# Kernel tuning notes

Hardware: AMD Instinct MI355X
Metric: run time of the kernel (lower is better)

The kernel has to match this reference:

```python
import jax, jax.numpy as jnp
import numpy as np

B, S, IN_DIM, D, H, L, C = 8, 1024, 256, 1024, 16, 6, 10
DK = D // H
EPS = 1e-5


def setup_inputs() -> dict:
    key = jax.random.key(0)
    ks = iter(jax.random.split(key, 64))
    n = lambda shape, s=0.02: jax.random.normal(next(ks), shape, dtype=jnp.float32) * s
    inp = {
        'x': jax.random.normal(next(ks), (B, S, IN_DIM), dtype=jnp.float32),
        'emb_w': n((IN_DIM, D)), 'emb_b': jnp.zeros((D,), jnp.float32),
        'Wq': n((L, D, D)), 'bq': jnp.zeros((L, D), jnp.float32),
        'Wk': n((L, D, D)), 'bk': jnp.zeros((L, D), jnp.float32),
        'Wv': n((L, D, D)), 'bv': jnp.zeros((L, D), jnp.float32),
        'Wo': n((L, D, D)), 'bo': jnp.zeros((L, D), jnp.float32),
        'W1': n((L, D, 4 * D)), 'b1': jnp.zeros((L, 4 * D), jnp.float32),
        'W2': n((L, 4 * D, D)), 'b2': jnp.zeros((L, D), jnp.float32),
        'ln1_s': jnp.ones((L, D), jnp.float32), 'ln1_b': jnp.zeros((L, D), jnp.float32),
        'ln2_s': jnp.ones((L, D), jnp.float32), 'ln2_b': jnp.zeros((L, D), jnp.float32),
        'fc_w': n((D, C)), 'fc_b': jnp.zeros((C,), jnp.float32),
    }
    return inp


def _pos_encoding_rows(n_rows):
    # Faithful to the torch module: pe is [max_len,1,D]; pe[:x.size(0)] picks the
    # first `batch` positions and broadcasts over the sequence dim.
    pos = jnp.arange(n_rows, dtype=jnp.float32)[:, None]
    div = jnp.exp(jnp.arange(0, D, 2, dtype=jnp.float32) * (-np.log(10000.0) / D))
    pe = jnp.zeros((n_rows, D), jnp.float32)
    pe = pe.at[:, 0::2].set(jnp.sin(pos * div)).at[:, 1::2].set(jnp.cos(pos * div))
    return pe


def _layer_norm(x, scale, bias):
    mu = jnp.mean(x, axis=-1, keepdims=True)
    var = jnp.mean(jnp.square(x - mu), axis=-1, keepdims=True)
    return (x - mu) * jax.lax.rsqrt(var + EPS) * scale + bias


def reference(x, emb_w, emb_b, Wq, bq, Wk, bk, Wv, bv, Wo, bo,
              W1, b1, W2, b2, ln1_s, ln1_b, ln2_s, ln2_b, fc_w, fc_b):
    h = x @ emb_w + emb_b                              # [B,S,D]
    h = h + _pos_encoding_rows(B)[:, None, :]          # broadcast pe[:B] over seq
    scale = 1.0 / np.sqrt(DK)
    for i in range(L):
        def heads(y, W, b):
            return (y @ W + b).reshape(B, S, H, DK).transpose(0, 2, 1, 3)  # bhsd
        q = heads(h, Wq[i], bq[i])
        k = heads(h, Wk[i], bk[i])
        v = heads(h, Wv[i], bv[i])
        scores = jnp.einsum('bhqd,bhkd->bhqk', q, k) * scale
        p = jax.nn.softmax(scores, axis=-1)
        o = jnp.einsum('bhqk,bhkd->bhqd', p, v)
        o = o.transpose(0, 2, 1, 3).reshape(B, S, D)
        attn_out = o @ Wo[i] + bo[i]
        h = _layer_norm(h + attn_out, ln1_s[i], ln1_b[i])
        ff = jax.nn.relu(h @ W1[i] + b1[i]) @ W2[i] + b2[i]
        h = _layer_norm(h + ff, ln2_s[i], ln2_b[i])
    pooled = jnp.mean(h, axis=1)                       # [B,D]
    return pooled @ fc_w + fc_b                        # [B,C]
```

## Files before the change

kernel.cpp:

```cpp
#include <hip/hip_runtime.h>
#include <stdint.h>

#define B_   8
#define S_   1024
#define IND  256
#define D_   1024
#define H_   16
#define DKH  64
#define L_   6
#define FF   4096
#define NTOK (B_*S_)

typedef __bf16 bf16;
typedef __attribute__((ext_vector_type(4))) float  f32x4;
typedef __attribute__((ext_vector_type(8))) __bf16 bf16x8;
typedef __attribute__((ext_vector_type(4))) __bf16 bf16x4;
typedef __attribute__((ext_vector_type(2))) __bf16 bf16x2;

#define AS1 __attribute__((address_space(1)))
#define AS3 __attribute__((address_space(3)))

__device__ __forceinline__ void gload16(const void* g, void* l) {
  __builtin_amdgcn_global_load_lds((AS1 void*)(const_cast<void*>(g)), (AS3 void*)l, 16, 0, 0);
}

__global__ __launch_bounds__(256)
void k_trans(const float* __restrict__ in, bf16* __restrict__ out,
             int K, int N, long inStride, long outStride) {
  __shared__ float t[32][33];
  const float* inp = in + (long)blockIdx.z * inStride;
  bf16* outp = out + (long)blockIdx.z * outStride;
  const int n0 = blockIdx.x * 32, k0 = blockIdx.y * 32;
  const int tx = threadIdx.x & 31, ty = threadIdx.x >> 5;
  #pragma unroll
  for (int j = 0; j < 32; j += 8)
    t[ty + j][tx] = inp[(long)(k0 + ty + j) * N + n0 + tx];
  __syncthreads();
  #pragma unroll
  for (int j = 0; j < 32; j += 8)
    outp[(long)(n0 + ty + j) * K + k0 + tx] = (bf16)t[tx][ty + j];
}

__global__ __launch_bounds__(256)
void k_f2b(const float* __restrict__ in, bf16* __restrict__ out) {
  const long i = ((long)blockIdx.x * 256 + threadIdx.x) * 4;
  f32x4 v = *(const f32x4*)(in + i);
  bf16x4 o;
  #pragma unroll
  for (int j = 0; j < 4; ++j) o[j] = (bf16)v[j];
  *(bf16x4*)(out + i) = o;
}

__global__ __launch_bounds__(256)
void k_pe(float* __restrict__ pe) {
  const int i = blockIdx.x * 256 + threadIdx.x;
  const int b = i >> 10, d = i & 1023;
  const float k2 = (float)(d & ~1);
  const float dv = __expf(k2 * (-9.210340371976184f / (float)D_));
  const float a = (float)b * dv;
  pe[i] = (d & 1) ? cosf(a) : sinf(a);
}

__global__ __launch_bounds__(256)
void k_packb(const float* __restrict__ bq, const float* __restrict__ bk,
             const float* __restrict__ bv, float* __restrict__ out) {
  const int i = blockIdx.x * 256 + threadIdx.x;
  const int l = i / 3072, j = i % 3072;
  const float* src = (j < 1024) ? bq : ((j < 2048) ? bk : bv);
  out[i] = src[l * 1024 + (j & 1023)];
}

template<int EPI>
__global__ __launch_bounds__(256)
void k_gemm(const bf16* __restrict__ A, const bf16* __restrict__ Bt,
            const float* __restrict__ bias,
            void* __restrict__ out0, void* __restrict__ out1,
            const float* __restrict__ pe,
            int M, int N, int K) {
  __shared__ __align__(16) bf16 sA[128 * 32];
  __shared__ __align__(16) bf16 sB[128 * 32];
  const int tid = threadIdx.x;
  const int lane = tid & 63, wv = tid >> 6;
  const int bx = blockIdx.x, by = blockIdx.y;
  const int wm = wv >> 1, wn = wv & 1;
  const int lg = lane >> 4, lc = lane & 15;
  const long arow0 = (long)by * 128;
  const long brow0 = (long)bx * 128;
  const int c0 = (wv * 2 + 0) * 64 + lane;
  const int c1 = (wv * 2 + 1) * 64 + lane;
  const int r0 = c0 >> 2, s0 = c0 & 3;
  const int r1 = c1 >> 2, s1 = c1 & 3;
  bf16* ldsA0 = sA + (wv * 2 + 0) * 512;
  bf16* ldsA1 = sA + (wv * 2 + 1) * 512;
  bf16* ldsB0 = sB + (wv * 2 + 0) * 512;
  bf16* ldsB1 = sB + (wv * 2 + 1) * 512;
  const bf16* Ab = A + arow0 * K;
  const bf16* Bb = Bt + brow0 * K;
  f32x4 acc[4][4] = {};
  const int kT = K >> 5;
  for (int kt = 0; kt < kT; ++kt) {
    const int k0 = kt << 5;
    gload16(Ab + (long)r0 * K + k0 + s0 * 8, ldsA0);
    gload16(Ab + (long)r1 * K + k0 + s1 * 8, ldsA1);
    gload16(Bb + (long)r0 * K + k0 + s0 * 8, ldsB0);
    gload16(Bb + (long)r1 * K + k0 + s1 * 8, ldsB1);
    __syncthreads();
    bf16x8 af[4], bfr[4];
    #pragma unroll
    for (int mr = 0; mr < 4; ++mr)
      af[mr] = *(const bf16x8*)(sA + (wm * 64 + mr * 16 + lc) * 32 + lg * 8);
    #pragma unroll
    for (int nc = 0; nc < 4; ++nc)
      bfr[nc] = *(const bf16x8*)(sB + (wn * 64 + nc * 16 + lc) * 32 + lg * 8);
    #pragma unroll
    for (int mr = 0; mr < 4; ++mr)
      #pragma unroll
      for (int nc = 0; nc < 4; ++nc)
        acc[mr][nc] = __builtin_amdgcn_mfma_f32_16x16x32_bf16(af[mr], bfr[nc], acc[mr][nc], 0, 0, 0);
    __syncthreads();
  }
  #pragma unroll
  for (int mr = 0; mr < 4; ++mr) {
    const int row0 = by * 128 + wm * 64 + mr * 16 + lg * 4;
    #pragma unroll
    for (int nc = 0; nc < 4; ++nc) {
      const int col = bx * 128 + wn * 64 + nc * 16 + lc;
      const float bv = bias[col];
      if constexpr (EPI == 2) {
        const int which = col >> 10;
        const int hh = (col & 1023) >> 6;
        const int dk = col & 63;
        const long bb = row0 >> 10;
        const int sr = row0 & 1023;
        if (which == 2) {
          bf16x4 pk;
          #pragma unroll
          for (int r = 0; r < 4; ++r) pk[r] = (bf16)(acc[mr][nc][r] + bv);
          *(bf16x4*)((bf16*)out1 + ((bb * H_ + hh) * (long)DKH + dk) * S_ + sr) = pk;
        } else {
          #pragma unroll
          for (int r = 0; r < 4; ++r) {
            float v = acc[mr][nc][r] + bv;
            if (which == 0) v *= 0.125f;
            ((bf16*)out0)[(long)which * NTOK * D_ + ((bb * H_ + hh) * (long)S_ + sr + r) * DKH + dk] = (bf16)v;
          }
        }
      } else {
        #pragma unroll
        for (int r = 0; r < 4; ++r) {
          float v = acc[mr][nc][r] + bv;
          const long rr = row0 + r;
          if constexpr (EPI == 0) {
            ((bf16*)out0)[rr * N + col] = (bf16)v;
          } else if constexpr (EPI == 1) {
            ((bf16*)out0)[rr * N + col] = (bf16)fmaxf(v, 0.f);
          } else {
            const long bb = rr >> 10;
            v += pe[bb * D_ + col];
            ((float*)out0)[rr * N + col] = v;
            ((bf16*)out1)[rr * N + col] = (bf16)v;
          }
        }
      }
    }
  }
}

__global__ __launch_bounds__(256)
void k_flash(const bf16* __restrict__ qg, const bf16* __restrict__ kgl,
             const bf16* __restrict__ vtg, bf16* __restrict__ og) {
  __shared__ __align__(16) bf16 sK[64 * 64];
  __shared__ __align__(16) bf16 sV[64 * 64];
  __shared__ __align__(16) bf16 sP[4 * 16 * 64];
  const int tid = threadIdx.x, lane = tid & 63, wv = tid >> 6;
  const int lg = lane >> 4, lc = lane & 15;
  const int bh = blockIdx.y, qt = blockIdx.x;
  const long base = (long)bh * S_ * DKH;
  const bf16* qb = qg + base;
  const bf16* kb = kgl + base;
  const bf16* vb = vtg + base;
  const int qrow = qt * 64 + wv * 16 + lc;
  const bf16x8 qf0 = *(const bf16x8*)(qb + (long)qrow * DKH + lg * 8);
  const bf16x8 qf1 = *(const bf16x8*)(qb + (long)qrow * DKH + 32 + lg * 8);
  float mrun = -3e38f, lrun = 0.f;
  f32x4 oacc[4] = {};
  bf16* sPw = sP + wv * (16 * 64);
  const int swzP = (lc & 7) << 4;
  const int c0 = wv * 128 + lane, c1 = c0 + 64;
  const int r0 = c0 >> 3, sl0 = (c0 & 7) ^ (r0 & 7);
  const int r1 = c1 >> 3, sl1 = (c1 & 7) ^ (r1 & 7);
  bf16* dst0 = sK + c0 * 8 - lane * 8;
  bf16* dst1 = sK + c1 * 8 - lane * 8;
  bf16* dstV0 = sV + c0 * 8 - lane * 8;
  bf16* dstV1 = sV + c1 * 8 - lane * 8;
  for (int kt = 0; kt < S_ / 64; ++kt) {
    const int gk = kt * 64;
    gload16(kb + (long)(gk + r0) * DKH + sl0 * 8, dst0);
    gload16(kb + (long)(gk + r1) * DKH + sl1 * 8, dst1);
    gload16(vb + (long)r0 * S_ + gk + sl0 * 8, dstV0);
    gload16(vb + (long)r1 * S_ + gk + sl1 * 8, dstV1);
    __syncthreads();
    f32x4 sacc[4] = {};
    #pragma unroll
    for (int nc = 0; nc < 4; ++nc) {
      const int kr = nc * 16 + lc;
      bf16x8 k0 = *(const bf16x8*)((char*)sK + kr * 128 + (((0 + lg) ^ (kr & 7)) << 4));
      bf16x8 k1 = *(const bf16x8*)((char*)sK + kr * 128 + (((4 + lg) ^ (kr & 7)) << 4));
      sacc[nc] = __builtin_amdgcn_mfma_f32_16x16x32_bf16(k0, qf0, sacc[nc], 0, 0, 0);
      sacc[nc] = __builtin_amdgcn_mfma_f32_16x16x32_bf16(k1, qf1, sacc[nc], 0, 0, 0);
    }
    float pm = sacc[0][0];
    #pragma unroll
    for (int nc = 0; nc < 4; ++nc)
      #pragma unroll
      for (int r = 0; r < 4; ++r) pm = fmaxf(pm, sacc[nc][r]);
    pm = fmaxf(pm, __shfl_xor(pm, 16));
    pm = fmaxf(pm, __shfl_xor(pm, 32));
    const float mnew = fmaxf(mrun, pm);
    const float fac = __expf(mrun - mnew);
    float ps = 0.f;
    #pragma unroll
    for (int nc = 0; nc < 4; ++nc)
      #pragma unroll
      for (int r = 0; r < 4; ++r) {
        const float p = __expf(sacc[nc][r] - mnew);
        sacc[nc][r] = p;
        ps += p;
      }
    ps += __shfl_xor(ps, 16);
    ps += __shfl_xor(ps, 32);
    lrun = lrun * fac + ps;
    mrun = mnew;
    #pragma unroll
    for (int nc = 0; nc < 4; ++nc)
      #pragma unroll
      for (int rp = 0; rp < 2; ++rp) {
        bf16x2 t;
        t[0] = (bf16)sacc[nc][rp * 2 + 0];
        t[1] = (bf16)sacc[nc][rp * 2 + 1];
        *(bf16x2*)((char*)sPw + lc * 128 + ((nc * 32 + lg * 8 + rp * 4) ^ swzP)) = t;
      }
    asm volatile("s_waitcnt lgkmcnt(0)" ::: "memory");
    __builtin_amdgcn_sched_barrier(0);
    float fr[4];
    #pragma unroll
    for (int r = 0; r < 4; ++r) fr[r] = __shfl(fac, lg * 4 + r);
    #pragma unroll
    for (int nc = 0; nc < 4; ++nc)
      #pragma unroll
      for (int r = 0; r < 4; ++r) oacc[nc][r] *= fr[r];
    #pragma unroll
    for (int m = 0; m < 2; ++m) {
      const bf16x8 pf = *(const bf16x8*)((char*)sPw + lc * 128 + ((m * 64 + lg * 16) ^ swzP));
      #pragma unroll
      for (int nc = 0; nc < 4; ++nc) {
        const int vr = nc * 16 + lc;
        bf16x8 vf = *(const bf16x8*)((char*)sV + vr * 128 + (((m * 4 + lg) ^ (vr & 7)) << 4));
        oacc[nc] = __builtin_amdgcn_mfma_f32_16x16x32_bf16(pf, vf, oacc[nc], 0, 0, 0);
      }
    }
    __syncthreads();
  }
  const int b = bh >> 4, h = bh & 15;
  const float linv = 1.f / lrun;
  #pragma unroll
  for (int r = 0; r < 4; ++r) {
    const float inv = __shfl(linv, lg * 4 + r);
    const int s = qt * 64 + wv * 16 + lg * 4 + r;
    const long obase = (((long)b * S_ + s) * H_ + h) * DKH;
    #pragma unroll
    for (int nc = 0; nc < 4; ++nc)
      og[obase + nc * 16 + lc] = (bf16)(oacc[nc][r] * inv);
  }
}

__global__ __launch_bounds__(256)
void k_addln(const float* __restrict__ hin, const bf16* __restrict__ dlt,
             const float* __restrict__ sc, const float* __restrict__ bi,
             float* __restrict__ hout, bf16* __restrict__ hbout) {
  const int row = blockIdx.x, t = threadIdx.x;
  const long off = (long)row * D_ + t * 4;
  f32x4 hv = *(const f32x4*)(hin + off);
  bf16x4 dv = *(const bf16x4*)(dlt + off);
  f32x4 x;
  float s = 0.f, ss = 0.f;
  #pragma unroll
  for (int j = 0; j < 4; ++j) { x[j] = hv[j] + (float)dv[j]; s += x[j]; ss += x[j] * x[j]; }
  #pragma unroll
  for (int m = 1; m < 64; m <<= 1) { s += __shfl_xor(s, m); ss += __shfl_xor(ss, m); }
  __shared__ float red[8];
  const int w = t >> 6, ln = t & 63;
  if (ln == 0) { red[w] = s; red[4 + w] = ss; }
  __syncthreads();
  s = red[0] + red[1] + red[2] + red[3];
  ss = red[4] + red[5] + red[6] + red[7];
  const float mu = s * (1.f / D_);
  const float rstd = rsqrtf(ss * (1.f / D_) - mu * mu + 1e-5f);
  f32x4 scv = *(const f32x4*)(sc + t * 4);
  f32x4 biv = *(const f32x4*)(bi + t * 4);
  f32x4 y; bf16x4 yb;
  #pragma unroll
  for (int j = 0; j < 4; ++j) { y[j] = (x[j] - mu) * rstd * scv[j] + biv[j]; yb[j] = (bf16)y[j]; }
  *(f32x4*)(hout + off) = y;
  *(bf16x4*)(hbout + off) = yb;
}

__global__ __launch_bounds__(256)
void k_pool1(const float* __restrict__ h, float* __restrict__ part) {
  const int i = blockIdx.x * 256 + threadIdx.x;
  const int b = i >> 10, d = i & 1023;
  const int s0 = blockIdx.y * 128;
  float s = 0.f;
  for (int t = 0; t < 128; ++t) s += h[((long)b * S_ + s0 + t) * D_ + d];
  part[(long)blockIdx.y * NTOK + i] = s;
}

__global__ __launch_bounds__(256)
void k_pool2(const float* __restrict__ part, float* __restrict__ pooled) {
  const int i = blockIdx.x * 256 + threadIdx.x;
  float s = 0.f;
  #pragma unroll
  for (int j = 0; j < 8; ++j) s += part[(long)j * NTOK + i];
  pooled[i] = s * (1.f / S_);
}

__global__ __launch_bounds__(64)
void k_fc(const float* __restrict__ pooled, const float* __restrict__ fw,
          const float* __restrict__ fb, float* __restrict__ out) {
  const int b = blockIdx.x / 10, c = blockIdx.x % 10;
  const int lane = threadIdx.x;
  float s = 0.f;
  for (int d = lane; d < D_; d += 64) s += pooled[b * D_ + d] * fw[d * 10 + c];
  #pragma unroll
  for (int m = 1; m < 64; m <<= 1) s += __shfl_xor(s, m);
  if (lane == 0) out[b * 10 + c] = s + fb[c];
}

extern "C" void kernel_launch(void* const* d_in, const int* in_sizes, int n_in,
                              void* d_out, int out_size, void* d_ws, size_t ws_size,
                              hipStream_t stream) {
  const float* x     = (const float*)d_in[0];
  const float* emb_w = (const float*)d_in[1];
  const float* emb_b = (const float*)d_in[2];
  const float* Wq    = (const float*)d_in[3];
  const float* bq    = (const float*)d_in[4];
  const float* Wk    = (const float*)d_in[5];
  const float* bk    = (const float*)d_in[6];
  const float* Wv    = (const float*)d_in[7];
  const float* bv    = (const float*)d_in[8];
  const float* Wo    = (const float*)d_in[9];
  const float* bo    = (const float*)d_in[10];
  const float* W1    = (const float*)d_in[11];
  const float* b1    = (const float*)d_in[12];
  const float* W2    = (const float*)d_in[13];
  const float* b2    = (const float*)d_in[14];
  const float* ln1s  = (const float*)d_in[15];
  const float* ln1b  = (const float*)d_in[16];
  const float* ln2s  = (const float*)d_in[17];
  const float* ln2b  = (const float*)d_in[18];
  const float* fcw   = (const float*)d_in[19];
  const float* fcb   = (const float*)d_in[20];

  char* w = (char*)d_ws;
  size_t off = 0;
  auto alloc = [&](size_t bytes) -> char* {
    char* p = w + off;
    off += (bytes + 255) & ~(size_t)255;
    return p;
  };
  bf16*  x_bf  = (bf16*) alloc((size_t)NTOK * IND * 2);
  bf16*  embT  = (bf16*) alloc((size_t)D_ * IND * 2);
  bf16*  qkvT  = (bf16*) alloc((size_t)L_ * 3 * D_ * D_ * 2);
  bf16*  woT   = (bf16*) alloc((size_t)L_ * D_ * D_ * 2);
  bf16*  w1T   = (bf16*) alloc((size_t)L_ * FF * D_ * 2);
  bf16*  w2T   = (bf16*) alloc((size_t)L_ * D_ * FF * 2);
  float* qkvB  = (float*)alloc((size_t)L_ * 3 * D_ * 4);
  float* pe    = (float*)alloc((size_t)B_ * D_ * 4);
  float* h_f   = (float*)alloc((size_t)NTOK * D_ * 4);
  bf16*  h_b   = (bf16*) alloc((size_t)NTOK * D_ * 2);
  bf16*  delta = (bf16*) alloc((size_t)NTOK * D_ * 2);
  float* pooled= (float*)alloc((size_t)B_ * D_ * 4);
  float* part  = (float*)alloc((size_t)8 * NTOK * 4);
  bf16*  scratch = (bf16*)alloc((size_t)NTOK * FF * 2);
  bf16* qb  = scratch;
  bf16* kb  = scratch + (size_t)NTOK * D_;
  bf16* vTb = scratch + (size_t)2 * NTOK * D_;
  bf16* ob  = scratch + (size_t)3 * NTOK * D_;
  bf16* ffn1 = scratch;
  (void)ws_size; (void)in_sizes; (void)n_in; (void)out_size;

  k_f2b<<<dim3(NTOK * IND / 1024), dim3(256), 0, stream>>>(x, x_bf);
  k_trans<<<dim3(D_ / 32, IND / 32, 1), dim3(256), 0, stream>>>(emb_w, embT, IND, D_, 0, 0);
  k_trans<<<dim3(32, 32, L_), dim3(256), 0, stream>>>(Wq, qkvT,               D_, D_, (long)D_ * D_, (long)3 * D_ * D_);
  k_trans<<<dim3(32, 32, L_), dim3(256), 0, stream>>>(Wk, qkvT + D_ * D_,     D_, D_, (long)D_ * D_, (long)3 * D_ * D_);
  k_trans<<<dim3(32, 32, L_), dim3(256), 0, stream>>>(Wv, qkvT + 2 * D_ * D_, D_, D_, (long)D_ * D_, (long)3 * D_ * D_);
  k_trans<<<dim3(32, 32, L_), dim3(256), 0, stream>>>(Wo, woT, D_, D_, (long)D_ * D_, (long)D_ * D_);
  k_trans<<<dim3(FF / 32, 32, L_), dim3(256), 0, stream>>>(W1, w1T, D_, FF, (long)D_ * FF, (long)FF * D_);
  k_trans<<<dim3(32, FF / 32, L_), dim3(256), 0, stream>>>(W2, w2T, FF, D_, (long)FF * D_, (long)D_ * FF);
  k_pe<<<dim3(B_ * D_ / 256), dim3(256), 0, stream>>>(pe);
  k_packb<<<dim3(L_ * 3 * D_ / 256), dim3(256), 0, stream>>>(bq, bk, bv, qkvB);

  k_gemm<3><<<dim3(D_ / 128, NTOK / 128), dim3(256), 0, stream>>>(
      x_bf, embT, emb_b, h_f, h_b, pe, NTOK, D_, IND);

  for (int l = 0; l < L_; ++l) {
    k_gemm<2><<<dim3(3 * D_ / 128, NTOK / 128), dim3(256), 0, stream>>>(
        h_b, qkvT + (size_t)l * 3 * D_ * D_, qkvB + l * 3 * D_,
        qb, vTb, nullptr, NTOK, 3 * D_, D_);
    k_flash<<<dim3(S_ / 64, B_ * H_), dim3(256), 0, stream>>>(qb, kb, vTb, ob);
    k_gemm<0><<<dim3(D_ / 128, NTOK / 128), dim3(256), 0, stream>>>(
        ob, woT + (size_t)l * D_ * D_, bo + l * D_,
        delta, nullptr, nullptr, NTOK, D_, D_);
    k_addln<<<dim3(NTOK), dim3(256), 0, stream>>>(h_f, delta, ln1s + l * D_, ln1b + l * D_, h_f, h_b);
    k_gemm<1><<<dim3(FF / 128, NTOK / 128), dim3(256), 0, stream>>>(
        h_b, w1T + (size_t)l * FF * D_, b1 + l * FF,
        ffn1, nullptr, nullptr, NTOK, FF, D_);
    k_gemm<0><<<dim3(D_ / 128, NTOK / 128), dim3(256), 0, stream>>>(
        ffn1, w2T + (size_t)l * D_ * FF, b2 + l * D_,
        delta, nullptr, nullptr, NTOK, D_, FF);
    k_addln<<<dim3(NTOK), dim3(256), 0, stream>>>(h_f, delta, ln2s + l * D_, ln2b + l * D_, h_f, h_b);
  }

  k_pool1<<<dim3(NTOK / 256, 8), dim3(256), 0, stream>>>(h_f, part);
  k_pool2<<<dim3(NTOK / 256), dim3(256), 0, stream>>>(part, pooled);
  k_fc<<<dim3(B_ * 10), dim3(64), 0, stream>>>(pooled, fcw, fcb, (float*)d_out);
}
```

Baseline: 2.661 ms.

## Add 256x256 tiled GEMM with ping-pong LDS pipelining for layer matmuls

Adds a new 512-thread GEMM kernel that computes 256x256 output tiles with double-buffered LDS fed by direct global-to-LDS loads. Loads are interleaved with MFMA phases using explicit vmcnt waits, barriers and setprio. All per-layer GEMMs (QKV, Wo, FFN1, FFN2) move to it, while the old kernel keeps only the embedding epilogue. The aim is more operand reuse per tile and better overlap of memory traffic with matrix math, at the cost of heavier register and LDS use. The larger tiles also mean fewer blocks, which risks lower occupancy (the Wo/FFN2 grids have only 128 blocks).

```diff
diff --git a/kernel.cpp b/kernel.cpp
--- a/kernel.cpp
+++ b/kernel.cpp
@@ -125,7 +125,123 @@
     #pragma unroll
     for (int nc = 0; nc < 4; ++nc) {
       const int col = bx * 128 + wn * 64 + nc * 16 + lc;
-      const float bv = bias[col];
+      const float bvv = bias[col];
+      #pragma unroll
+      for (int r = 0; r < 4; ++r) {
+        float v = acc[mr][nc][r] + bvv;
+        const long rr = row0 + r;
+        if constexpr (EPI == 0) {
+          ((bf16*)out0)[rr * N + col] = (bf16)v;
+        } else {
+          const long bb = rr >> 10;
+          v += pe[bb * D_ + col];
+          ((float*)out0)[rr * N + col] = v;
+          ((bf16*)out1)[rr * N + col] = (bf16)v;
+        }
+      }
+    }
+  }
+}
+
+template<int EPI>
+__global__ __launch_bounds__(512, 2)
+void k_gemm256(const bf16* __restrict__ A, const bf16* __restrict__ Bt,
+               const float* __restrict__ bias,
+               void* __restrict__ out0, void* __restrict__ out1,
+               int M, int N, int K) {
+  __shared__ __align__(16) bf16 lds[65536];
+  const int tid = threadIdx.x;
+  const int lane = tid & 63, wv = tid >> 6;
+  const int wm = wv >> 2, wn = wv & 3;
+  const int lg = lane >> 4, lc = lane & 15;
+  const int tileRow = blockIdx.y * 256, tileCol = blockIdx.x * 256;
+  const bf16* Abase = A + (long)tileRow * K;
+  const bf16* Bbase = Bt + (long)tileCol * K;
+  const long laneOff = (long)lc * K + lg * 8;
+  f32x4 acc[8][4] = {};
+  const int NT = K >> 6;
+  const int NI = NT >> 1;
+
+  auto stA = [&](int t, int h, int bb) {
+    const int rg = h * 16 + wv * 2;
+    const int mb = rg >> 1;
+    const bf16* s = Abase + (long)(mb * 16) * K + t * 64 + laneOff;
+    bf16* d = lds + bb * 32768 + rg * 512;
+    gload16(s, d);
+    gload16(s + 32, d + 512);
+  };
+  auto stB = [&](int t, int h, int bb) {
+    const int rg = h * 16 + wv * 2;
+    const int mb = rg >> 1;
+    const bf16* s = Bbase + (long)(mb * 16) * K + t * 64 + laneOff;
+    bf16* d = lds + bb * 32768 + 16384 + rg * 512;
+    gload16(s, d);
+    gload16(s + 32, d + 512);
+  };
+
+  bf16x8 aF[8];
+  bf16x8 bF0[4], bF1[4];
+
+#define LDA(BB, MH) do { _Pragma("unroll") for (int m = 0; m < 4; ++m) \
+    _Pragma("unroll") for (int kk = 0; kk < 2; ++kk) \
+      aF[m*2+kk] = *(const bf16x8*)(lds + (BB)*32768 + ((wm*8 + (MH)*4 + m)*2 + kk)*512 + lane*8); \
+  } while(0)
+#define LDB(BB, NH, DST) do { _Pragma("unroll") for (int n = 0; n < 2; ++n) \
+    _Pragma("unroll") for (int kk = 0; kk < 2; ++kk) \
+      DST[n*2+kk] = *(const bf16x8*)(lds + (BB)*32768 + 16384 + ((wn*4 + (NH)*2 + n)*2 + kk)*512 + lane*8); \
+  } while(0)
+#define MM(MH, NH, BSRC, VM) do { \
+    if ((VM) == 1) asm volatile("s_waitcnt vmcnt(4)" ::: "memory"); \
+    if ((VM) == 2) asm volatile("s_waitcnt vmcnt(0)" ::: "memory"); \
+    __builtin_amdgcn_s_barrier(); \
+    __builtin_amdgcn_s_setprio(1); \
+    _Pragma("unroll") for (int m = 0; m < 4; ++m) \
+      _Pragma("unroll") for (int n = 0; n < 2; ++n) { \
+        acc[(MH)*4+m][(NH)*2+n] = __builtin_amdgcn_mfma_f32_16x16x32_bf16(aF[m*2+0], BSRC[n*2+0], acc[(MH)*4+m][(NH)*2+n], 0, 0, 0); \
+        acc[(MH)*4+m][(NH)*2+n] = __builtin_amdgcn_mfma_f32_16x16x32_bf16(aF[m*2+1], BSRC[n*2+1], acc[(MH)*4+m][(NH)*2+n], 0, 0, 0); \
+      } \
+    __builtin_amdgcn_s_setprio(0); \
+    __builtin_amdgcn_s_barrier(); \
+  } while(0)
+
+  stA(0, 0, 0); stB(0, 0, 0); stA(0, 1, 0); stB(0, 1, 0);
+  if (NT > 1) { stA(1, 0, 1); stB(1, 0, 1); }
+  asm volatile("s_waitcnt vmcnt(4)" ::: "memory");
+  __builtin_amdgcn_s_barrier();
+
+  for (int i = 0; i < NI - 1; ++i) {
+    const int t1 = 2 * i + 1, t2 = 2 * i + 2, t3 = 2 * i + 3;
+    LDA(0, 0); LDB(0, 0, bF0); stA(t1, 1, 1); MM(0, 0, bF0, 0);
+    LDB(0, 1, bF1);            stB(t1, 1, 1); MM(0, 1, bF1, 0);
+    LDA(0, 1);                 stA(t2, 0, 0); MM(1, 0, bF0, 0);
+                               stB(t2, 0, 0); MM(1, 1, bF1, 1);
+    LDA(1, 0); LDB(1, 0, bF0); stA(t2, 1, 0); MM(0, 0, bF0, 0);
+    LDB(1, 1, bF1);            stB(t2, 1, 0); MM(0, 1, bF1, 0);
+    LDA(1, 1);                 stA(t3, 0, 1); MM(1, 0, bF0, 0);
+                               stB(t3, 0, 1); MM(1, 1, bF1, 1);
+  }
+  {
+    const int t1 = NT - 1;
+    LDA(0, 0); LDB(0, 0, bF0); stA(t1, 1, 1); MM(0, 0, bF0, 0);
+    LDB(0, 1, bF1);            stB(t1, 1, 1); MM(0, 1, bF1, 0);
+    LDA(0, 1);                                MM(1, 0, bF0, 0);
+                                              MM(1, 1, bF1, 2);
+    LDA(1, 0); LDB(1, 0, bF0);                MM(0, 0, bF0, 0);
+    LDB(1, 1, bF1);                           MM(0, 1, bF1, 0);
+    LDA(1, 1);                                MM(1, 0, bF0, 0);
+                                              MM(1, 1, bF1, 0);
+  }
+#undef LDA
+#undef LDB
+#undef MM
+
+  #pragma unroll
+  for (int mr = 0; mr < 8; ++mr) {
+    const int row0 = tileRow + wm * 128 + mr * 16 + lg * 4;
+    #pragma unroll
+    for (int nr = 0; nr < 4; ++nr) {
+      const int col = tileCol + wn * 64 + nr * 16 + lc;
+      const float bvv = bias[col];
       if constexpr (EPI == 2) {
         const int which = col >> 10;
         const int hh = (col & 1023) >> 6;
@@ -135,12 +251,12 @@
         if (which == 2) {
           bf16x4 pk;
           #pragma unroll
-          for (int r = 0; r < 4; ++r) pk[r] = (bf16)(acc[mr][nc][r] + bv);
+          for (int r = 0; r < 4; ++r) pk[r] = (bf16)(acc[mr][nr][r] + bvv);
           *(bf16x4*)((bf16*)out1 + ((bb * H_ + hh) * (long)DKH + dk) * S_ + sr) = pk;
         } else {
           #pragma unroll
           for (int r = 0; r < 4; ++r) {
-            float v = acc[mr][nc][r] + bv;
+            float v = acc[mr][nr][r] + bvv;
             if (which == 0) v *= 0.125f;
             ((bf16*)out0)[(long)which * NTOK * D_ + ((bb * H_ + hh) * (long)S_ + sr + r) * DKH + dk] = (bf16)v;
           }
@@ -148,18 +264,10 @@
       } else {
         #pragma unroll
         for (int r = 0; r < 4; ++r) {
-          float v = acc[mr][nc][r] + bv;
+          float v = acc[mr][nr][r] + bvv;
           const long rr = row0 + r;
-          if constexpr (EPI == 0) {
-            ((bf16*)out0)[rr * N + col] = (bf16)v;
-          } else if constexpr (EPI == 1) {
-            ((bf16*)out0)[rr * N + col] = (bf16)fmaxf(v, 0.f);
-          } else {
-            const long bb = rr >> 10;
-            v += pe[bb * D_ + col];
-            ((float*)out0)[rr * N + col] = v;
-            ((bf16*)out1)[rr * N + col] = (bf16)v;
-          }
+          if constexpr (EPI == 1) v = fmaxf(v, 0.f);
+          ((bf16*)out0)[rr * N + col] = (bf16)v;
         }
       }
     }
@@ -404,20 +512,20 @@
       x_bf, embT, emb_b, h_f, h_b, pe, NTOK, D_, IND);
 
   for (int l = 0; l < L_; ++l) {
-    k_gemm<2><<<dim3(3 * D_ / 128, NTOK / 128), dim3(256), 0, stream>>>(
+    k_gemm256<2><<<dim3(3 * D_ / 256, NTOK / 256), dim3(512), 0, stream>>>(
         h_b, qkvT + (size_t)l * 3 * D_ * D_, qkvB + l * 3 * D_,
-        qb, vTb, nullptr, NTOK, 3 * D_, D_);
+        qb, vTb, NTOK, 3 * D_, D_);
     k_flash<<<dim3(S_ / 64, B_ * H_), dim3(256), 0, stream>>>(qb, kb, vTb, ob);
-    k_gemm<0><<<dim3(D_ / 128, NTOK / 128), dim3(256), 0, stream>>>(
+    k_gemm256<0><<<dim3(D_ / 256, NTOK / 256), dim3(512), 0, stream>>>(
         ob, woT + (size_t)l * D_ * D_, bo + l * D_,
-        delta, nullptr, nullptr, NTOK, D_, D_);
+        delta, nullptr, NTOK, D_, D_);
     k_addln<<<dim3(NTOK), dim3(256), 0, stream>>>(h_f, delta, ln1s + l * D_, ln1b + l * D_, h_f, h_b);
-    k_gemm<1><<<dim3(FF / 128, NTOK / 128), dim3(256), 0, stream>>>(
+    k_gemm256<1><<<dim3(FF / 256, NTOK / 256), dim3(512), 0, stream>>>(
         h_b, w1T + (size_t)l * FF * D_, b1 + l * FF,
-        ffn1, nullptr, nullptr, NTOK, FF, D_);
-    k_gemm<0><<<dim3(D_ / 128, NTOK / 128), dim3(256), 0, stream>>>(
+        ffn1, nullptr, NTOK, FF, D_);
+    k_gemm256<0><<<dim3(D_ / 256, NTOK / 256), dim3(512), 0, stream>>>(
         ffn1, w2T + (size_t)l * D_ * FF, b2 + l * D_,
-        delta, nullptr, nullptr, NTOK, D_, FF);
+        delta, nullptr, NTOK, D_, FF);
     k_addln<<<dim3(NTOK), dim3(256), 0, stream>>>(h_f, delta, ln2s + l * D_, ln2b + l * D_, h_f, h_b);
   }
 
```

Result: no change. 2.656 ms (-0.2%).
